# Kernel optimization log

Measured on AMD Instinct MI355X. Metric: run time of the kernel, lower is better.

The kernel has to match this reference:

```python
import jax, jax.numpy as jnp
import numpy as np

T, B, C, H, W = 9, 8, 256, 56, 56


def setup_inputs() -> dict:
    key = jax.random.key(0)
    k1, k2, k3, k4 = jax.random.split(key, 4)
    feature_maps_sequence = jax.random.normal(k1, (T, B, C, H, W), dtype=jnp.float32)
    # Conv2d(2C, 1, kernel_size=1): weight [1, 2C, 1, 1], bias [1]
    w = jax.random.normal(k2, (1, 2 * C, 1, 1), dtype=jnp.float32) * 0.02
    b = jax.random.normal(k3, (1,), dtype=jnp.float32) * 0.02
    gamma = jax.random.normal(k4, (1,), dtype=jnp.float32)
    return {"feature_maps_sequence": feature_maps_sequence, "w": w, "b": b, "gamma": gamma}


def reference(feature_maps_sequence, w, b, gamma):
    seq = feature_maps_sequence  # [T, B, C, H, W]
    t = seq.shape[0]
    center = seq[t // 2]  # [B, C, H, W]
    c = seq.shape[2]
    # 1x1 conv over concat([center, frame]) == dot with split weight halves + bias
    w_center = w[0, :c, 0, 0]  # [C]
    w_other = w[0, c:, 0, 0]   # [C]
    score_center = jnp.einsum('bchw,c->bhw', center, w_center)          # [B, H, W]
    score_other = jnp.einsum('tbchw,c->tbhw', seq, w_other)             # [T, B, H, W]
    scores = score_center[None] + score_other + b[0]                    # [T, B, H, W]
    attn = jax.nn.softmax(scores, axis=0)                               # softmax over T
    attended = jnp.einsum('tbhw,tbchw->bchw', attn, seq)                # [B, C, H, W]
    return center + gamma * attended
```

## Files before the change

### kernel.cpp

```cpp
#include <hip/hip_runtime.h>
#include <math.h>

#define TT 9
#define BN 8
#define CC 256
#define HW 3136
#define P 4
#define NCHUNK (HW / P)
#define CENTER_T 4

__global__ __launch_bounds__(256, 4) void fused_stage_kernel(
    const float* __restrict__ seq, const float* __restrict__ w,
    const float* __restrict__ gamma, float* __restrict__ out) {
  const int blk = blockIdx.x;
  const int b = blk & 7;
  const int chunk = blk >> 3;
  const int px0 = chunk * P;
  const int tid = threadIdx.x;

  __shared__ __align__(16) float tile[TT * CC * P];
  __shared__ float wsh[CC];
  __shared__ __align__(16) float red[36 * 4];
  __shared__ __align__(16) float sc[TT * P];

  wsh[tid] = w[CC + tid];

  {
    const float* sgb = seq + ((size_t)b * CC + tid) * HW + px0;
    float4 pre[TT];
#pragma unroll
    for (int t = 0; t < TT; ++t)
      pre[t] = *(const float4*)(sgb + (size_t)t * (BN * CC * HW));
#pragma unroll
    for (int t = 0; t < TT; ++t)
      *(float4*)(&tile[(t * 1024 + 4 * tid) ^ ((t & 1) << 4)]) = pre[t];
  }
  __syncthreads();

  if (tid < 144) {
    const int cp = tid & 3;
    const int pair = tid >> 2;
    const int t = pair >> 2;
    const int px = pair & 3;
    const int e = t & 1;
    const int sbase = t * 1024 + 4 * cp + px;
    float a = 0.f;
#pragma unroll
    for (int j = 0; j < 64; ++j)
      a = fmaf(tile[sbase + 16 * j], wsh[cp + 4 * (j ^ e)], a);
    red[tid] = a;
  }
  __syncthreads();

  if (tid < P) {
    const int px = tid;
    float vv[TT];
    float m = -1e30f;
#pragma unroll
    for (int t = 0; t < TT; ++t) {
      const float4 r = *(const float4*)(&red[(t * 4 + px) * 4]);
      const float s = (r.x + r.y) + (r.z + r.w);
      vv[t] = s;
      m = fmaxf(m, s);
    }
    float s = 0.f;
#pragma unroll
    for (int t = 0; t < TT; ++t) { vv[t] = __expf(vv[t] - m); s += vv[t]; }
    const float inv = 1.f / s;
#pragma unroll
    for (int t = 0; t < TT; ++t) sc[t * P + px] = vv[t] * inv;
  }
  __syncthreads();

  {
    const int c = tid;
    float4 o = {0.f, 0.f, 0.f, 0.f};
    float4 cv = {0.f, 0.f, 0.f, 0.f};
#pragma unroll
    for (int t = 0; t < TT; ++t) {
      const float4 s = *(const float4*)(&sc[t * P]);
      const float4 v = *(const float4*)(&tile[(t * 1024 + 4 * c) ^ ((t & 1) << 4)]);
      o.x = fmaf(s.x, v.x, o.x);
      o.y = fmaf(s.y, v.y, o.y);
      o.z = fmaf(s.z, v.z, o.z);
      o.w = fmaf(s.w, v.w, o.w);
      if (t == CENTER_T) cv = v;
    }
    const float gm = gamma[0];
    float4 r;
    r.x = fmaf(gm, o.x, cv.x);
    r.y = fmaf(gm, o.y, cv.y);
    r.z = fmaf(gm, o.z, cv.z);
    r.w = fmaf(gm, o.w, cv.w);
    float* ob = out + ((size_t)b * CC + c) * HW + px0;
    *(float4*)(ob) = r;
  }
}

extern "C" void kernel_launch(void* const* d_in, const int* in_sizes, int n_in,
                              void* d_out, int out_size, void* d_ws, size_t ws_size,
                              hipStream_t stream) {
  const float* seq = (const float*)d_in[0];
  const float* w = (const float*)d_in[1];
  const float* gamma = (const float*)d_in[3];
  float* out = (float*)d_out;

  fused_stage_kernel<<<BN * NCHUNK, 256, 0, stream>>>(seq, w, gamma, out);
}
```

Before: 363.0 us.

## Stream pixel windows with coalesced loads and two-pass global reads instead of LDS tile

Each block now handles 32 contiguous pixels, with 8 threads per channel group reading contiguous float4s, instead of staging a 4-pixel tile of all channels in shared memory. The channel-weighted scores are accumulated in registers, reduced through shared memory, and then the sequence is re-read from global memory for the attention-weighted sum. This aims to improve memory coalescing and reduce LDS use, at the cost of reading the input twice and relying on cache for the second pass.

After: 371.4 us. +2.3%, slower.

```diff
diff --git a/kernel.cpp b/kernel.cpp
--- a/kernel.cpp
+++ b/kernel.cpp
@@ -5,61 +5,70 @@
 #define BN 8
 #define CC 256
 #define HW 3136
-#define P 4
-#define NCHUNK (HW / P)
+#define PX 32
+#define NW (HW / PX)
+#define CI 32
+#define CJ (CC / CI)
 #define CENTER_T 4
+#define PSTR (TT * PX + 4)
 
-__global__ __launch_bounds__(256, 4) void fused_stage_kernel(
+__global__ __launch_bounds__(256, 4) void fused_stream_kernel(
     const float* __restrict__ seq, const float* __restrict__ w,
     const float* __restrict__ gamma, float* __restrict__ out) {
   const int blk = blockIdx.x;
   const int b = blk & 7;
-  const int chunk = blk >> 3;
-  const int px0 = chunk * P;
+  const int wdw = blk >> 3;
+  const int px0 = wdw * PX;
   const int tid = threadIdx.x;
+  const int ci = tid >> 3;
+  const int ui = tid & 7;
 
-  __shared__ __align__(16) float tile[TT * CC * P];
-  __shared__ float wsh[CC];
-  __shared__ __align__(16) float red[36 * 4];
-  __shared__ __align__(16) float sc[TT * P];
+  __shared__ __align__(16) float part[CI * PSTR];
+  __shared__ float scr[TT * PX];
+  __shared__ __align__(16) float attn[TT * PX];
 
-  wsh[tid] = w[CC + tid];
+  float wreg[CJ];
+#pragma unroll
+  for (int j = 0; j < CJ; ++j) wreg[j] = w[CC + ci + CI * j];
 
-  {
-    const float* sgb = seq + ((size_t)b * CC + tid) * HW + px0;
-    float4 pre[TT];
+  const float* base0 = seq + ((size_t)b * CC + ci) * HW + px0 + 4 * ui;
+
+  float4 acc[TT];
 #pragma unroll
-    for (int t = 0; t < TT; ++t)
-      pre[t] = *(const float4*)(sgb + (size_t)t * (BN * CC * HW));
+  for (int t = 0; t < TT; ++t) acc[t] = make_float4(0.f, 0.f, 0.f, 0.f);
+
 #pragma unroll
-    for (int t = 0; t < TT; ++t)
-      *(float4*)(&tile[(t * 1024 + 4 * tid) ^ ((t & 1) << 4)]) = pre[t];
+  for (int j = 0; j < CJ; ++j) {
+    const float wj = wreg[j];
+#pragma unroll
+    for (int t = 0; t < TT; ++t) {
+      const float4 v =
+          *(const float4*)(base0 + (size_t)t * (BN * CC * HW) + (size_t)j * (CI * HW));
+      acc[t].x = fmaf(wj, v.x, acc[t].x);
+      acc[t].y = fmaf(wj, v.y, acc[t].y);
+      acc[t].z = fmaf(wj, v.z, acc[t].z);
+      acc[t].w = fmaf(wj, v.w, acc[t].w);
+    }
+  }
+#pragma unroll
+  for (int t = 0; t < TT; ++t)
+    *(float4*)(&part[ci * PSTR + t * PX + ui * 4]) = acc[t];
+  __syncthreads();
+
+  for (int v = tid; v < TT * PX; v += 256) {
+    float s = 0.f;
+#pragma unroll
+    for (int c2 = 0; c2 < CI; ++c2) s += part[c2 * PSTR + v];
+    scr[v] = s;
   }
   __syncthreads();
 
-  if (tid < 144) {
-    const int cp = tid & 3;
-    const int pair = tid >> 2;
-    const int t = pair >> 2;
-    const int px = pair & 3;
-    const int e = t & 1;
-    const int sbase = t * 1024 + 4 * cp + px;
-    float a = 0.f;
-#pragma unroll
-    for (int j = 0; j < 64; ++j)
-      a = fmaf(tile[sbase + 16 * j], wsh[cp + 4 * (j ^ e)], a);
-    red[tid] = a;
-  }
-  __syncthreads();
-
-  if (tid < P) {
-    const int px = tid;
+  if (tid < PX) {
     float vv[TT];
     float m = -1e30f;
 #pragma unroll
     for (int t = 0; t < TT; ++t) {
-      const float4 r = *(const float4*)(&red[(t * 4 + px) * 4]);
-      const float s = (r.x + r.y) + (r.z + r.w);
+      const float s = scr[t * PX + tid];
       vv[t] = s;
       m = fmaxf(m, s);
     }
@@ -68,31 +77,36 @@
     for (int t = 0; t < TT; ++t) { vv[t] = __expf(vv[t] - m); s += vv[t]; }
     const float inv = 1.f / s;
 #pragma unroll
-    for (int t = 0; t < TT; ++t) sc[t * P + px] = vv[t] * inv;
+    for (int t = 0; t < TT; ++t) attn[t * PX + tid] = vv[t] * inv;
   }
   __syncthreads();
 
-  {
-    const int c = tid;
-    float4 o = {0.f, 0.f, 0.f, 0.f};
-    float4 cv = {0.f, 0.f, 0.f, 0.f};
+  float4 at[TT];
+#pragma unroll
+  for (int t = 0; t < TT; ++t)
+    at[t] = *(const float4*)(&attn[t * PX + ui * 4]);
+
+  const float gm = gamma[0];
+#pragma unroll
+  for (int j = 0; j < CJ; ++j) {
+    float4 o = make_float4(0.f, 0.f, 0.f, 0.f);
+    float4 cv = make_float4(0.f, 0.f, 0.f, 0.f);
 #pragma unroll
     for (int t = 0; t < TT; ++t) {
-      const float4 s = *(const float4*)(&sc[t * P]);
-      const float4 v = *(const float4*)(&tile[(t * 1024 + 4 * c) ^ ((t & 1) << 4)]);
-      o.x = fmaf(s.x, v.x, o.x);
-      o.y = fmaf(s.y, v.y, o.y);
-      o.z = fmaf(s.z, v.z, o.z);
-      o.w = fmaf(s.w, v.w, o.w);
+      const float4 v =
+          *(const float4*)(base0 + (size_t)t * (BN * CC * HW) + (size_t)j * (CI * HW));
+      o.x = fmaf(at[t].x, v.x, o.x);
+      o.y = fmaf(at[t].y, v.y, o.y);
+      o.z = fmaf(at[t].z, v.z, o.z);
+      o.w = fmaf(at[t].w, v.w, o.w);
       if (t == CENTER_T) cv = v;
     }
-    const float gm = gamma[0];
     float4 r;
     r.x = fmaf(gm, o.x, cv.x);
     r.y = fmaf(gm, o.y, cv.y);
     r.z = fmaf(gm, o.z, cv.z);
     r.w = fmaf(gm, o.w, cv.w);
-    float* ob = out + ((size_t)b * CC + c) * HW + px0;
+    float* ob = out + ((size_t)b * CC + ci + CI * j) * HW + px0 + 4 * ui;
     *(float4*)(ob) = r;
   }
 }
@@ -105,5 +119,5 @@
   const float* gamma = (const float*)d_in[3];
   float* out = (float*)d_out;
 
-  fused_stage_kernel<<<BN * NCHUNK, 256, 0, stream>>>(seq, w, gamma, out);
+  fused_stream_kernel<<<BN * NW, 256, 0, stream>>>(seq, w, gamma, out);
 }
```

## Split fused kernel into coalesced scores, softmax and attend passes

Applied to the files above, without the earlier changes.

Replaces the single fused kernel, which loaded a 4-pixel tile per channel with strided 16-byte reads, with three kernels. A scores kernel does contiguous channel-group partial dot products into scratch stored in the output buffer. A softmax kernel reduces the partials and normalises over time into workspace. An attend kernel streams the sequence again with fully coalesced float4 loads, walking blocks in reverse order so recently read data may still be in cache. This trades a second full read of the input, plus extra launches, for much better memory coalescing.

Result: slower. 401.9 us (+10.7%).

```diff
diff --git a/kernel.cpp b/kernel.cpp
--- a/kernel.cpp
+++ b/kernel.cpp
@@ -5,96 +5,117 @@
 #define BN 8
 #define CC 256
 #define HW 3136
-#define P 4
-#define NCHUNK (HW / P)
+#define HW4 (HW / 4)
+#define CG 16
+#define CPG (CC / CG)
 #define CENTER_T 4
+#define TSTRIDE ((size_t)BN * CC * HW)
 
-__global__ __launch_bounds__(256, 4) void fused_stage_kernel(
+__global__ __launch_bounds__(256) void scores_kernel(
     const float* __restrict__ seq, const float* __restrict__ w,
-    const float* __restrict__ gamma, float* __restrict__ out) {
+    float* __restrict__ scratch) {
   const int blk = blockIdx.x;
-  const int b = blk & 7;
-  const int chunk = blk >> 3;
-  const int px0 = chunk * P;
+  const int t = blk >> 7;
+  const int b = (blk >> 4) & 7;
+  const int cg = blk & 15;
   const int tid = threadIdx.x;
 
-  __shared__ __align__(16) float tile[TT * CC * P];
-  __shared__ float wsh[CC];
-  __shared__ __align__(16) float red[36 * 4];
-  __shared__ __align__(16) float sc[TT * P];
-
-  wsh[tid] = w[CC + tid];
-
-  {
-    const float* sgb = seq + ((size_t)b * CC + tid) * HW + px0;
-    float4 pre[TT];
-#pragma unroll
-    for (int t = 0; t < TT; ++t)
-      pre[t] = *(const float4*)(sgb + (size_t)t * (BN * CC * HW));
-#pragma unroll
-    for (int t = 0; t < TT; ++t)
-      *(float4*)(&tile[(t * 1024 + 4 * tid) ^ ((t & 1) << 4)]) = pre[t];
-  }
+  __shared__ float wsh[CPG];
+  if (tid < CPG) wsh[tid] = w[CC + cg * CPG + tid];
   __syncthreads();
 
-  if (tid < 144) {
-    const int cp = tid & 3;
-    const int pair = tid >> 2;
-    const int t = pair >> 2;
-    const int px = pair & 3;
-    const int e = t & 1;
-    const int sbase = t * 1024 + 4 * cp + px;
-    float a = 0.f;
+  const float* base =
+      seq + (((size_t)t * BN + b) * CC + cg * CPG) * HW;
+
+  float4 acc[4];
 #pragma unroll
-    for (int j = 0; j < 64; ++j)
-      a = fmaf(tile[sbase + 16 * j], wsh[cp + 4 * (j ^ e)], a);
-    red[tid] = a;
+  for (int k = 0; k < 4; ++k) acc[k] = make_float4(0.f, 0.f, 0.f, 0.f);
+
+  for (int j = 0; j < CPG; ++j) {
+    const float wj = wsh[j];
+    const float* rp = base + (size_t)j * HW;
+#pragma unroll
+    for (int k = 0; k < 4; ++k) {
+      const int q = tid + 256 * k;
+      if (k < 3 || tid < HW4 - 768) {
+        const float4 v = *(const float4*)(rp + 4 * q);
+        acc[k].x = fmaf(wj, v.x, acc[k].x);
+        acc[k].y = fmaf(wj, v.y, acc[k].y);
+        acc[k].z = fmaf(wj, v.z, acc[k].z);
+        acc[k].w = fmaf(wj, v.w, acc[k].w);
+      }
+    }
   }
-  __syncthreads();
+  float* op = scratch + (size_t)blk * HW;
+#pragma unroll
+  for (int k = 0; k < 4; ++k) {
+    const int q = tid + 256 * k;
+    if (k < 3 || tid < HW4 - 768) *(float4*)(op + 4 * q) = acc[k];
+  }
+}
 
-  if (tid < P) {
-    const int px = tid;
-    float vv[TT];
-    float m = -1e30f;
+__global__ __launch_bounds__(256) void softmax_kernel(
+    const float* __restrict__ scratch, float* __restrict__ attn) {
+  const int i = blockIdx.x * 256 + threadIdx.x;
+  if (i >= BN * HW) return;
+  const int b = i / HW;
+  const int px = i - b * HW;
+
+  float sc[TT];
+  float m = -1e30f;
 #pragma unroll
-    for (int t = 0; t < TT; ++t) {
-      const float4 r = *(const float4*)(&red[(t * 4 + px) * 4]);
-      const float s = (r.x + r.y) + (r.z + r.w);
-      vv[t] = s;
-      m = fmaxf(m, s);
-    }
+  for (int t = 0; t < TT; ++t) {
     float s = 0.f;
 #pragma unroll
-    for (int t = 0; t < TT; ++t) { vv[t] = __expf(vv[t] - m); s += vv[t]; }
-    const float inv = 1.f / s;
+    for (int cg = 0; cg < CG; ++cg)
+      s += scratch[(size_t)((t * BN + b) * CG + cg) * HW + px];
+    sc[t] = s;
+    m = fmaxf(m, s);
+  }
+  float sum = 0.f;
 #pragma unroll
-    for (int t = 0; t < TT; ++t) sc[t * P + px] = vv[t] * inv;
+  for (int t = 0; t < TT; ++t) { sc[t] = __expf(sc[t] - m); sum += sc[t]; }
+  const float inv = 1.f / sum;
+#pragma unroll
+  for (int t = 0; t < TT; ++t)
+    attn[(size_t)(t * BN + b) * HW + px] = sc[t] * inv;
+}
+
+__global__ __launch_bounds__(256) void attend_kernel(
+    const float* __restrict__ seq, const float* __restrict__ attn,
+    const float* __restrict__ gamma, float* __restrict__ out) {
+  const int rb = gridDim.x - 1 - blockIdx.x;
+  const int i = rb * 256 + threadIdx.x;
+  const int b = i / (CC * HW4);
+  const int rem = i - b * (CC * HW4);
+  const int c = rem / HW4;
+  const int q = rem - c * HW4;
+
+  const float* sp = seq + ((size_t)b * CC + c) * HW + 4 * q;
+  const float* ap = attn + (size_t)b * HW + 4 * q;
+
+  float4 v[TT], a[TT];
+#pragma unroll
+  for (int t = 0; t < TT; ++t) v[t] = *(const float4*)(sp + t * TSTRIDE);
+#pragma unroll
+  for (int t = 0; t < TT; ++t)
+    a[t] = *(const float4*)(ap + (size_t)t * (BN * HW));
+
+  float4 o = make_float4(0.f, 0.f, 0.f, 0.f);
+#pragma unroll
+  for (int t = 0; t < TT; ++t) {
+    o.x = fmaf(a[t].x, v[t].x, o.x);
+    o.y = fmaf(a[t].y, v[t].y, o.y);
+    o.z = fmaf(a[t].z, v[t].z, o.z);
+    o.w = fmaf(a[t].w, v[t].w, o.w);
   }
-  __syncthreads();
-
-  {
-    const int c = tid;
-    float4 o = {0.f, 0.f, 0.f, 0.f};
-    float4 cv = {0.f, 0.f, 0.f, 0.f};
-#pragma unroll
-    for (int t = 0; t < TT; ++t) {
-      const float4 s = *(const float4*)(&sc[t * P]);
-      const float4 v = *(const float4*)(&tile[(t * 1024 + 4 * c) ^ ((t & 1) << 4)]);
-      o.x = fmaf(s.x, v.x, o.x);
-      o.y = fmaf(s.y, v.y, o.y);
-      o.z = fmaf(s.z, v.z, o.z);
-      o.w = fmaf(s.w, v.w, o.w);
-      if (t == CENTER_T) cv = v;
-    }
-    const float gm = gamma[0];
-    float4 r;
-    r.x = fmaf(gm, o.x, cv.x);
-    r.y = fmaf(gm, o.y, cv.y);
-    r.z = fmaf(gm, o.z, cv.z);
-    r.w = fmaf(gm, o.w, cv.w);
-    float* ob = out + ((size_t)b * CC + c) * HW + px0;
-    *(float4*)(ob) = r;
-  }
+  const float gm = gamma[0];
+  float4 r;
+  r.x = fmaf(gm, o.x, v[CENTER_T].x);
+  r.y = fmaf(gm, o.y, v[CENTER_T].y);
+  r.z = fmaf(gm, o.z, v[CENTER_T].z);
+  r.w = fmaf(gm, o.w, v[CENTER_T].w);
+  *(float4*)(out + ((size_t)b * CC + c) * HW + 4 * q) = r;
 }
 
 extern "C" void kernel_launch(void* const* d_in, const int* in_sizes, int n_in,
@@ -104,6 +125,10 @@
   const float* w = (const float*)d_in[1];
   const float* gamma = (const float*)d_in[3];
   float* out = (float*)d_out;
+  float* attn = (float*)d_ws;
+  float* scratch = out;
 
-  fused_stage_kernel<<<BN * NCHUNK, 256, 0, stream>>>(seq, w, gamma, out);
+  scores_kernel<<<TT * BN * CG, 256, 0, stream>>>(seq, w, scratch);
+  softmax_kernel<<<(BN * HW + 255) / 256, 256, 0, stream>>>(scratch, attn);
+  attend_kernel<<<(BN * CC * HW4) / 256, 256, 0, stream>>>(seq, attn, gamma, out);
 }
```
